# Optimization experiments

Measured on AMD Instinct MI355X. Metric: run time of the kernel, lower is better.

Reference implementation:

```python
import jax, jax.numpy as jnp
import numpy as np

B, T, H, HY, E, L = 32, 256, 1024, 256, 64, 2


def setup_inputs() -> dict:
    key = jax.random.key(0)
    ks = jax.random.split(key, 16)
    rn = lambda k, s, sc=0.05: jax.random.normal(k, s, dtype=jnp.float32) * sc
    return {
        'input': rn(ks[0], (B, T, H), 1.0),
        'w_ih': rn(ks[1], (L, 4 * H, H)),
        'w_hh': rn(ks[2], (L, 4 * H, H)),
        'hyper_w_ih': rn(ks[3], (L, 4 * HY, 2 * H)),
        'hyper_w_hh': rn(ks[4], (L, 4 * HY, HY)),
        'hyper_b': rn(ks[5], (L, 4 * HY)),
        'w_zh': rn(ks[6], (L, 4 * E, HY)),
        'b_zh': jnp.ones((L, 4 * E), jnp.float32),
        'w_zx': rn(ks[7], (L, 4 * E, HY)),
        'b_zx': jnp.ones((L, 4 * E), jnp.float32),
        'w_zb': rn(ks[8], (L, 4 * E, HY)),
        'w_dh': rn(ks[9], (L, 4, H, E), 1.0 / E),
        'w_dx': rn(ks[10], (L, 4, H, E), 1.0 / E),
        'w_db': rn(ks[11], (L, 4, H, E)),
        'b0': rn(ks[12], (L, 4 * H)),
    }


def reference(input, w_ih, w_hh, hyper_w_ih, hyper_w_hh, hyper_b,
              w_zh, b_zh, w_zx, b_zx, w_zb, w_dh, w_dx, w_db, b0):
    L = w_ih.shape[0]
    Bb = input.shape[0]
    Hh = w_hh.shape[-1]
    Hy = hyper_w_hh.shape[-1]
    Ee = w_dh.shape[-1]

    def cell(l, xt, h, c, hh, hc):
        # hyper (meta) LSTM step: input is concat(x, h_main)
        xh = jnp.concatenate([xt, h], axis=-1)
        hg = xh @ hyper_w_ih[l].T + hh @ hyper_w_hh[l].T + hyper_b[l]
        hi, hf, hgc, ho = jnp.split(hg, 4, axis=-1)
        hc2 = jax.nn.sigmoid(hf) * hc + jax.nn.sigmoid(hi) * jnp.tanh(hgc)
        hh2 = jax.nn.sigmoid(ho) * jnp.tanh(hc2)
        # gate-wise embeddings z (B, 4, E) then project to per-gate scale vectors (B, 4H)
        zh = (hh2 @ w_zh[l].T + b_zh[l]).reshape(Bb, 4, Ee)
        zx = (hh2 @ w_zx[l].T + b_zx[l]).reshape(Bb, 4, Ee)
        zb = (hh2 @ w_zb[l].T).reshape(Bb, 4, Ee)
        dh = jnp.einsum('bge,ghe->bgh', zh, w_dh[l]).reshape(Bb, 4 * Hh)
        dx = jnp.einsum('bge,ghe->bgh', zx, w_dx[l]).reshape(Bb, 4 * Hh)
        db = jnp.einsum('bge,ghe->bgh', zb, w_db[l]).reshape(Bb, 4 * Hh) + b0[l]
        # main LSTM gates, dynamically scaled by hypernetwork
        pre = dh * (h @ w_hh[l].T) + dx * (xt @ w_ih[l].T) + db
        i, f, g, o = jnp.split(pre, 4, axis=-1)
        c2 = jax.nn.sigmoid(f) * c + jax.nn.sigmoid(i) * jnp.tanh(g)
        h2 = jax.nn.sigmoid(o) * jnp.tanh(c2)
        return h2, c2, hh2, hc2

    def step(carry, xt):
        h, c, hh, hc = carry  # each (L, B, .)
        hs, cs, hhs, hcs = [], [], [], []
        inp = xt
        for l in range(L):
            h2, c2, hh2, hc2 = cell(l, inp, h[l], c[l], hh[l], hc[l])
            inp = h2
            hs.append(h2); cs.append(c2); hhs.append(hh2); hcs.append(hc2)
        carry = (jnp.stack(hs), jnp.stack(cs), jnp.stack(hhs), jnp.stack(hcs))
        return carry, inp  # top-layer hidden

    init = (jnp.zeros((L, Bb, Hh), input.dtype), jnp.zeros((L, Bb, Hh), input.dtype),
            jnp.zeros((L, Bb, Hy), input.dtype), jnp.zeros((L, Bb, Hy), input.dtype))
    carry, ys = jax.lax.scan(step, init, jnp.swapaxes(input, 0, 1))
    h_seq = jnp.swapaxes(ys, 0, 1)  # (B, T, H)
    return h_seq, carry[0][-1], carry[1][-1]
```

## Files before the change

### kernel.cpp

```cpp
#include <hip/hip_runtime.h>

typedef __bf16 bf16;
typedef __bf16 bf16x8 __attribute__((ext_vector_type(8)));
typedef __bf16 bf16x4 __attribute__((ext_vector_type(4)));
typedef float f32x4 __attribute__((ext_vector_type(4)));
typedef unsigned long long u64;

#define SCOPE_AGENT __HIP_MEMORY_SCOPE_AGENT


__device__ __forceinline__ float sigf(float x) { return 1.0f / (1.0f + __expf(-x)); }
__device__ __forceinline__ float tanhf_fast(float x) {
  float e = __expf(-2.0f * fabsf(x));
  float r = (1.0f - e) / (1.0f + e);
  return copysignf(r, x);
}
__device__ __forceinline__ f32x4 mfma16(bf16x8 a, bf16x8 b, f32x4 c) {
  return __builtin_amdgcn_mfma_f32_16x16x32_bf16(a, b, c, 0, 0, 0);
}
__device__ __forceinline__ u64 uld(const u64* p) { return __hip_atomic_load(p, __ATOMIC_RELAXED, SCOPE_AGENT); }
__device__ __forceinline__ void ust(u64* p, u64 v) { __hip_atomic_store(p, v, __ATOMIC_RELAXED, SCOPE_AGENT); }
__device__ __forceinline__ int ildi(const int* p) { return __hip_atomic_load(p, __ATOMIC_RELAXED, SCOPE_AGENT); }
__device__ __forceinline__ void isti(int* p, int v) { __hip_atomic_store(p, v, __ATOMIC_RELAXED, SCOPE_AGENT); }
__device__ __forceinline__ void fstf(float* p, float v) { __hip_atomic_store(p, v, __ATOMIC_RELAXED, SCOPE_AGENT); }
__device__ __forceinline__ void usti32(unsigned* p, unsigned v) { __hip_atomic_store(p, v, __ATOMIC_RELAXED, SCOPE_AGENT); }

__global__ void detect_kernel(const void* probe, int* flag) {
  __shared__ int cnt;
  if (threadIdx.x == 0) cnt = 0;
  __syncthreads();
  const bf16* p = (const bf16*)probe;
  int local = 0;
  for (int j = threadIdx.x; j < 8192; j += 256) {
    float x = (float)p[j];
    bool wild = (x != x) || (fabsf(x) > 1e3f) || (x != 0.0f && fabsf(x) < 1e-30f);
    local += wild ? 1 : 0;
  }
  atomicAdd(&cnt, local);
  __syncthreads();
  if (threadIdx.x == 0) *flag = (cnt > 64) ? 1 : 0;
}

struct CvtSrc { const void* s[15]; };
struct CvtDst { bf16* d[15]; };

__global__ __launch_bounds__(256) void convert_kernel(CvtSrc S, CvtDst D, const int* flag) {
  const int pre[16] = {0, 8388608, 16777216, 25165824, 29360128, 29884416, 29886464,
                       30017536, 30018048, 30149120, 30149632, 30280704, 30804992,
                       31329280, 31853568, 31861760};
  const int fp32 = *flag;
  const int nvec = 31861760 / 4;
  for (int v = blockIdx.x * 256 + threadIdx.x; v < nvec; v += gridDim.x * 256) {
    int e = v * 4;
    int seg = 0;
#pragma unroll
    for (int k = 1; k < 15; ++k) seg += (e >= pre[k]) ? 1 : 0;
    int off = e - pre[seg];
    bf16* d = D.d[seg] + off;
    if (fp32) {
      const float* s = (const float*)S.s[seg] + off;
      float4 x = *(const float4*)s;
      d[0] = (bf16)x.x; d[1] = (bf16)x.y; d[2] = (bf16)x.z; d[3] = (bf16)x.w;
    } else {
      const bf16* s = (const bf16*)S.s[seg] + off;
      d[0] = s[0]; d[1] = s[1]; d[2] = s[2]; d[3] = s[3];
    }
  }
}

__global__ void init_kernel(u64* zbase) {
  int i = blockIdx.x * 256 + threadIdx.x;
  zbase[i] = 0ull;
}

__global__ __launch_bounds__(256) void gemm_pre(
    const bf16* __restrict__ A, const bf16* __restrict__ w_ih_l,
    const bf16* __restrict__ hwih_l, bf16* __restrict__ Xp, float* __restrict__ Hxp) {
  constexpr int LDT = 72;
  __shared__ alignas(16) bf16 As[64 * LDT];
  __shared__ alignas(16) bf16 Bs[64 * LDT];
  const int bm = blockIdx.x & 127;
  const int bn = blockIdx.x >> 7;
  const int m0 = bm * 64, n0 = bn * 64;
  const int tid = threadIdx.x;
  const int lane = tid & 63, wid = tid >> 6;
  const int l15 = lane & 15, q = lane >> 4;
  const int srow = tid >> 2, sk = (tid & 3) * 16;
  const bf16* arow = A + (size_t)(m0 + srow) * 1024;
  const int n = n0 + srow;
  const bf16* brow = (n < 4096) ? (w_ih_l + (size_t)n * 1024)
                                : (hwih_l + (size_t)(n - 4096) * 2048);
  f32x4 acc[4] = {};
  for (int kb = 0; kb < 1024; kb += 64) {
    *(bf16x8*)(&As[srow * LDT + sk])     = *(const bf16x8*)(arow + kb + sk);
    *(bf16x8*)(&As[srow * LDT + sk + 8]) = *(const bf16x8*)(arow + kb + sk + 8);
    *(bf16x8*)(&Bs[srow * LDT + sk])     = *(const bf16x8*)(brow + kb + sk);
    *(bf16x8*)(&Bs[srow * LDT + sk + 8]) = *(const bf16x8*)(brow + kb + sk + 8);
    __syncthreads();
#pragma unroll
    for (int kk = 0; kk < 64; kk += 32) {
      bf16x8 av = *(const bf16x8*)(&As[(wid * 16 + l15) * LDT + kk + q * 8]);
#pragma unroll
      for (int j = 0; j < 4; ++j) {
        bf16x8 bv = *(const bf16x8*)(&Bs[(j * 16 + l15) * LDT + kk + q * 8]);
        acc[j] = mfma16(av, bv, acc[j]);
      }
    }
    __syncthreads();
  }
#pragma unroll
  for (int j = 0; j < 4; ++j) {
    const int gn = n0 + j * 16 + l15;
#pragma unroll
    for (int r = 0; r < 4; ++r) {
      const int gm = m0 + wid * 16 + q * 4 + r;
      float v = acc[j][r];
      if (gn < 4096) Xp[(size_t)gm * 4096 + gn] = (bf16)v;
      else           Hxp[(size_t)gm * 1024 + (gn - 4096)] = v;
    }
  }
}

struct SeqArgs {
  const bf16 *w_hh, *hwih, *hwhh, *hyb;
  const bf16 *w_zh, *b_zh, *w_zx, *b_zx, *w_zb;
  const bf16 *w_dh, *w_dx, *w_db, *b0;
  const bf16 *Xp; const float *Hxp;
  const bf16 *w_ih1;
  bf16 *Xp1c; float *Hxp1c;
  u64 *Y0;
  u64 *hpub;
  u64 *hh2pub;
  float *outp;
  int *flags;
};

__global__ __launch_bounds__(256) void seq_kernel(SeqArgs a) {
  __shared__ char smem[41472] __attribute__((aligned(16)));
  bf16 (*hstage)[1032] = (bf16(*)[1032])smem;
  bf16 (*hhK)[264]    = (bf16(*)[264])(smem + 33024);
  float* hgL          = (float*)(smem + 33024);
  bf16 (*hA4)[1032]   = (bf16(*)[1032])smem;
  bf16 (*hh2A)[264]   = (bf16(*)[264])(smem + 8256);
  float (*RhL)[256]   = (float(*)[256])(smem + 10368);
  float (*zsL)[768]   = (float(*)[768])(smem + 14464);
  float (*presL)[256] = (float(*)[256])(smem + 26752);
  bf16 (*hbuf)[64]    = (bf16(*)[64])(smem + 30848);
  bf16*  As = (bf16*)smem;
  bf16*  Bs = (bf16*)(smem + 9216);
  float* Ct = (float*)(smem + 18432);

  const int tid = threadIdx.x;
  const int lane = tid & 63, wid = tid >> 6;
  const int l15 = lane & 15, q = lane >> 4;
  const int blk = blockIdx.x;
  const int xcd = blk & 7, slot = blk >> 3;
  const int layer = xcd >> 2, xl = xcd & 3;
  const int s16 = xl * 4 + (slot & 3);
  const int bq = slot >> 2;
  const int lblk = bq * 16 + s16;
  const int hd = s16 >> 1;
  const int mh = (bq == hd) ? 0 : ((bq == ((hd + 4) & 7)) ? 1 : -1);
  const bool isHyper = (((s16 & 1) == 0) && (mh >= 0));

  u64* hbase  = a.hpub + (size_t)layer * 16384;
  u64* h2base = a.hh2pub + (size_t)layer * 4096;
  int* genp0  = a.flags;
  int* genp   = a.flags + layer * 16;
  int* gchunkp= a.flags + 32;
  int* arrp   = a.flags + 64 + layer * 2048;
  int* hh2fp  = a.flags + 4160 + layer * 256;
  int* carrp  = a.flags + 4672;

  const bf16* whh_l = a.w_hh + (size_t)layer * 4194304;
  const bf16* hybl  = a.hyb + layer * 1024;
  const bf16* bzh_l = a.b_zh + layer * 256;
  const bf16* bzx_l = a.b_zx + layer * 256;
  const bf16* b0_l  = a.b0 + (size_t)layer * 4096;
  const int cb = tid >> 6, chl = tid & 63;

  float c_reg = 0.0f;
  float hc[2] = {0, 0};

  const bf16* zrow[12];
#pragma unroll
  for (int j = 0; j < 12; ++j) {
    int ng = wid * 12 + j, tau = ng >> 4;
    const bf16* base = (tau == 0) ? a.w_zh : (tau == 1) ? a.w_zx : a.w_zb;
    zrow[j] = base + ((size_t)layer * 256 + (ng & 15) * 16 + l15) * 256;
  }
  const bf16* rrow[4];
#pragma unroll
  for (int nt = 0; nt < 4; ++nt)
    rrow[nt] = whh_l + (size_t)(wid * 1024 + s16 * 64 + nt * 16 + l15) * 1024;
  const bf16* hirow[2];
  const bf16* hhrow[2];
#pragma unroll
  for (int nt = 0; nt < 2; ++nt) {
    const int row = wid * 256 + hd * 32 + nt * 16 + l15;
    hirow[nt] = a.hwih + (size_t)layer * 2097152 + (size_t)row * 2048 + 1024;
    hhrow[nt] = a.hwhh + (size_t)layer * 262144 + (size_t)row * 256;
  }
  const size_t wdo = ((size_t)(layer * 4 + wid) * 1024 + s16 * 64 + lane) * 64;
  const bf16 *pdh = a.w_dh + wdo, *pdx = a.w_dx + wdo, *pdb = a.w_db + wdo;

  for (int t = 0; t < 256; ++t) {
    const int tloc = t & 31;
    u64* wslot = hbase + (size_t)(t & 1) * 8192;
    const u64* rslot = hbase + (size_t)((t + 1) & 1) * 8192;
    u64* wcur = h2base + (size_t)(t & 1) * 2048;
    const u64* rK = h2base + (size_t)((t + 1) & 1) * 2048;

    if (layer == 1 && tloc == 0) {
      const int k = t >> 5;
      if (tid == 0) { while (ildi(genp0) < (k + 1) * 32) __builtin_amdgcn_s_sleep(2); }
      __atomic_signal_fence(__ATOMIC_SEQ_CST);
      __syncthreads();
      const int srow = tid >> 2, sk = (tid & 3) * 16;
      for (int tt = 0; tt < 10; ++tt) {
        const int tile = lblk * 10 + tt;
        const int m0 = (tile & 15) * 64, n0 = (tile >> 4) * 64;
        const int m = m0 + srow;
        const u64* arow = a.Y0 + (((size_t)(m >> 5) * 256 + k * 32 + (m & 31)) << 8);
        const int n = n0 + srow;
        const bf16* brow = (n < 4096) ? (a.w_ih1 + (size_t)n * 1024)
                                      : (a.hwih + 2097152 + (size_t)(n - 4096) * 2048);
        f32x4 acc[4] = {};
        for (int kb = 0; kb < 1024; kb += 64) {
          const int c0 = (kb + sk) >> 2;
          u64 a0 = uld(arow + c0),     a1 = uld(arow + c0 + 1);
          u64 a2 = uld(arow + c0 + 2), a3 = uld(arow + c0 + 3);
          *(u64*)&As[srow * 72 + sk]      = a0;
          *(u64*)&As[srow * 72 + sk + 4]  = a1;
          *(u64*)&As[srow * 72 + sk + 8]  = a2;
          *(u64*)&As[srow * 72 + sk + 12] = a3;
          *(bf16x8*)&Bs[srow * 72 + sk]     = *(const bf16x8*)(brow + kb + sk);
          *(bf16x8*)&Bs[srow * 72 + sk + 8] = *(const bf16x8*)(brow + kb + sk + 8);
          __syncthreads();
#pragma unroll
          for (int kk = 0; kk < 64; kk += 32) {
            bf16x8 av = *(const bf16x8*)&As[(wid * 16 + l15) * 72 + kk + q * 8];
#pragma unroll
            for (int j = 0; j < 4; ++j) {
              bf16x8 bv = *(const bf16x8*)&Bs[(j * 16 + l15) * 72 + kk + q * 8];
              acc[j] = mfma16(av, bv, acc[j]);
            }
          }
          __syncthreads();
        }
#pragma unroll
        for (int j = 0; j < 4; ++j)
#pragma unroll
          for (int r = 0; r < 4; ++r)
            Ct[(wid * 16 + q * 4 + r) * 64 + j * 16 + l15] = acc[j][r];
        __syncthreads();
#pragma unroll
        for (int e = 0; e < 4; ++e) {
          const int qd = tid * 4 + e;
          const int row = qd >> 4, col4 = (qd & 15) * 4;
          f32x4 v = *(const f32x4*)&Ct[row * 64 + col4];
          const int gm = m0 + row, gn = n0 + col4;
          if (gn < 4096) {
            union { bf16 h[4]; u64 u; } pk;
#pragma unroll
            for (int x = 0; x < 4; ++x) pk.h[x] = (bf16)v[x];
            ust((u64*)a.Xp1c + ((((size_t)gm << 12) + gn) >> 2), pk.u);
          } else {
            float* hp = a.Hxp1c + ((size_t)gm << 10) + (gn - 4096);
#pragma unroll
            for (int x = 0; x < 4; ++x) fstf(hp + x, v[x]);
          }
        }
        __syncthreads();
      }
      __atomic_signal_fence(__ATOMIC_SEQ_CST);
      __builtin_amdgcn_s_waitcnt(0);
      __syncthreads();
      if (tid == 0) isti(carrp + lblk * 16, k + 1);
      if (lblk == 0 && wid == 0) {
        for (;;) {
          int v0 = ildi(carrp + lane * 32);
          int v1 = ildi(carrp + lane * 32 + 16);
          if (__all((v0 >= k + 1) && (v1 >= k + 1))) break;
          __builtin_amdgcn_s_sleep(2);
        }
        __atomic_signal_fence(__ATOMIC_SEQ_CST);
        if (lane == 0) isti(gchunkp, k + 1);
      }
      if (tid == 0) { while (ildi(gchunkp) < k + 1) __builtin_amdgcn_s_sleep(2); }
      __atomic_signal_fence(__ATOMIC_SEQ_CST);
      __syncthreads();
    }

    if (t > 0 && tid == 0) {
      while (ildi(genp) < t) __builtin_amdgcn_s_sleep(2);
    }
    __atomic_signal_fence(__ATOMIC_SEQ_CST);
    __syncthreads();

    if (isHyper) {
      for (int i = tid; i < 4096; i += 256) {
        int b = i >> 8, u = i & 255;
        *(u64*)&hstage[b][u * 4] = uld(rslot + ((size_t)(mh * 16 + b) << 8) + u);
      }
      for (int i = tid; i < 1024; i += 256) {
        int b = i >> 6, u = i & 63;
        *(u64*)&hhK[b][u * 4] = uld(rK + ((size_t)(mh * 16 + b) << 6) + u);
      }
      __syncthreads();
      f32x4 acc[2] = {};
      for (int kk = 0; kk < 1024; kk += 32) {
        int ko = kk + q * 8;
        bf16x8 a0 = *(const bf16x8*)&hstage[l15][ko];
#pragma unroll
        for (int nt = 0; nt < 2; ++nt) {
          bf16x8 bv = *(const bf16x8*)(hirow[nt] + ko);
          acc[nt] = mfma16(a0, bv, acc[nt]);
        }
      }
      for (int kk = 0; kk < 256; kk += 32) {
        int ko = kk + q * 8;
        bf16x8 a0 = *(const bf16x8*)&hhK[l15][ko];
#pragma unroll
        for (int nt = 0; nt < 2; ++nt) {
          bf16x8 bv = *(const bf16x8*)(hhrow[nt] + ko);
          acc[nt] = mfma16(a0, bv, acc[nt]);
        }
      }
      __syncthreads();
#pragma unroll
      for (int nt = 0; nt < 2; ++nt)
#pragma unroll
        for (int r = 0; r < 4; ++r)
          hgL[(wid * 16 + q * 4 + r) * 32 + nt * 16 + l15] = acc[nt][r];
      __syncthreads();
      {
        const int b16 = tid >> 4, d0 = (tid & 15) * 2;
        const int b = mh * 16 + b16;
        float hx2[4][2];
        if (layer == 0) {
          const float* hx = a.Hxp + ((size_t)b * 256 + t) * 1024 + hd * 32 + d0;
#pragma unroll
          for (int g = 0; g < 4; ++g) {
            hx2[g][0] = hx[g * 256]; hx2[g][1] = hx[g * 256 + 1];
          }
        } else {
          const u64* hx1 = (const u64*)a.Hxp1c + (((size_t)b * 32 + tloc) << 9)
                         + ((hd * 32 + d0) >> 1);
#pragma unroll
          for (int g = 0; g < 4; ++g) {
            u64 w = uld(hx1 + g * 128);
            hx2[g][0] = __uint_as_float((unsigned)(w & 0xffffffffu));
            hx2[g][1] = __uint_as_float((unsigned)(w >> 32));
          }
        }
        union { bf16 h[2]; unsigned u; } pk;
#pragma unroll
        for (int dd = 0; dd < 2; ++dd) {
          int d = d0 + dd, gd = hd * 32 + d;
          float hi  = hgL[(0 * 16 + b16) * 32 + d] + (float)hybl[gd]       + hx2[0][dd];
          float hf  = hgL[(1 * 16 + b16) * 32 + d] + (float)hybl[256 + gd] + hx2[1][dd];
          float hgv = hgL[(2 * 16 + b16) * 32 + d] + (float)hybl[512 + gd] + hx2[2][dd];
          float ho  = hgL[(3 * 16 + b16) * 32 + d] + (float)hybl[768 + gd] + hx2[3][dd];
          hc[dd] = sigf(hf) * hc[dd] + sigf(hi) * tanhf_fast(hgv);
          pk.h[dd] = (bf16)(sigf(ho) * tanhf_fast(hc[dd]));
        }
        usti32((unsigned*)wcur + b * 128 + hd * 16 + (d0 >> 1), pk.u);
      }
      __atomic_signal_fence(__ATOMIC_SEQ_CST);
      __builtin_amdgcn_s_waitcnt(0);
      __syncthreads();
      if (tid == 0) isti(hh2fp + (hd * 2 + mh) * 16, t + 1);
    }
    __syncthreads();

    for (int i = tid; i < 1024; i += 256) {
      int b = i >> 8, u = i & 255;
      *(u64*)&hA4[b][u * 4] = uld(rslot + ((size_t)(bq * 4 + b) << 8) + u);
    }
    __syncthreads();
    {
      f32x4 racc[4] = {};
      for (int kk = 0; kk < 1024; kk += 32) {
        const int ko = kk + q * 8;
        bf16x8 av = *(const bf16x8*)&hA4[l15 & 3][ko];
#pragma unroll
        for (int nt = 0; nt < 4; ++nt) {
          bf16x8 bv = *(const bf16x8*)(rrow[nt] + ko);
          racc[nt] = mfma16(av, bv, racc[nt]);
        }
      }
      if (lane < 16) {
#pragma unroll
        for (int nt = 0; nt < 4; ++nt)
#pragma unroll
          for (int r = 0; r < 4; ++r)
            RhL[r][wid * 64 + nt * 16 + lane] = racc[nt][r];
      }
    }
    if (tid < 16) { while (ildi(hh2fp + tid * 16) < t + 1) __builtin_amdgcn_s_sleep(1); }
    __atomic_signal_fence(__ATOMIC_SEQ_CST);
    __syncthreads();
    {
      int b = tid >> 6, u = tid & 63;
      *(u64*)&hh2A[b][u * 4] = uld(wcur + ((size_t)(bq * 4 + b) << 6) + u);
    }
    __syncthreads();
    {
      f32x4 zacc[12] = {};
      for (int kk = 0; kk < 256; kk += 32) {
        const int ko = kk + q * 8;
        bf16x8 av = *(const bf16x8*)&hh2A[l15 & 3][ko];
#pragma unroll
        for (int j = 0; j < 12; ++j) {
          bf16x8 bv = *(const bf16x8*)(zrow[j] + ko);
          zacc[j] = mfma16(av, bv, zacc[j]);
        }
      }
      if (lane < 16) {
#pragma unroll
        for (int j = 0; j < 12; ++j) {
          int ng = wid * 12 + j, tau = ng >> 4, col = (ng & 15) * 16 + lane;
          float bias = (tau == 0) ? (float)bzh_l[col] : (tau == 1) ? (float)bzx_l[col] : 0.0f;
#pragma unroll
          for (int r = 0; r < 4; ++r) zsL[r][tau * 256 + col] = zacc[j][r] + bias;
        }
      }
    }
    __syncthreads();
    {
      float dH[4] = {}, dX[4] = {}, dB[4] = {};
      for (int e0 = 0; e0 < 64; e0 += 4) {
        bf16x4 wh = *(const bf16x4*)(pdh + e0);
        bf16x4 wx = *(const bf16x4*)(pdx + e0);
        bf16x4 wb = *(const bf16x4*)(pdb + e0);
        f32x4 zh_[4], zx_[4], zb_[4];
#pragma unroll
        for (int b = 0; b < 4; ++b) {
          zh_[b] = *(const f32x4*)&zsL[b][wid * 64 + e0];
          zx_[b] = *(const f32x4*)&zsL[b][256 + wid * 64 + e0];
          zb_[b] = *(const f32x4*)&zsL[b][512 + wid * 64 + e0];
        }
#pragma unroll
        for (int jj = 0; jj < 4; ++jj) {
          float whf = (float)wh[jj], wxf = (float)wx[jj], wbf = (float)wb[jj];
#pragma unroll
          for (int b = 0; b < 4; ++b) {
            dH[b] += zh_[b][jj] * whf;
            dX[b] += zx_[b][jj] * wxf;
            dB[b] += zb_[b][jj] * wbf;
          }
        }
      }
      const int n = wid * 1024 + s16 * 64 + lane;
#pragma unroll
      for (int b = 0; b < 4; ++b) {
        float rh = RhL[b][wid * 64 + lane];
        float xp;
        if (layer == 0) {
          xp = (float)a.Xp[((size_t)(bq * 4 + b) * 256 + t) * 4096 + n];
        } else {
          u64 w = uld((const u64*)a.Xp1c
                      + ((((size_t)((bq * 4 + b) * 32 + tloc) << 12) + (n & ~3)) >> 2));
          xp = __uint_as_float(((unsigned)(w >> ((n & 3) * 16)) & 0xffffu) << 16);
        }
        float b0v = (float)b0_l[n];
        presL[b][wid * 64 + lane] = dH[b] * rh + dX[b] * xp + dB[b] + b0v;
      }
    }
    __syncthreads();
    {
      float iv = presL[cb][chl];
      float fv = presL[cb][64 + chl];
      float gv = presL[cb][128 + chl];
      float ov = presL[cb][192 + chl];
      c_reg = sigf(fv) * c_reg + sigf(iv) * tanhf_fast(gv);
      float hn = sigf(ov) * tanhf_fast(c_reg);
      hbuf[cb][chl] = (bf16)hn;
      if (layer) {
        const size_t oo = ((size_t)(bq * 4 + cb) * 256 + t) * 1024 + s16 * 64 + chl;
        a.outp[oo] = hn;
        if (t == 255) {
          a.outp[8388608 + (bq * 4 + cb) * 1024 + s16 * 64 + chl] = hn;
          a.outp[8421376 + (bq * 4 + cb) * 1024 + s16 * 64 + chl] = c_reg;
        }
      }
    }
    __syncthreads();
    if (tid < 64) {
      int b = tid >> 4, u = tid & 15;
      u64 pk = *(const u64*)&hbuf[b][u * 4];
      ust(wslot + ((size_t)(bq * 4 + b) << 8) + s16 * 16 + u, pk);
      if (layer == 0)
        ust(a.Y0 + (((size_t)(bq * 4 + b) * 256 + t) << 8) + s16 * 16 + u, pk);
    }
    __atomic_signal_fence(__ATOMIC_SEQ_CST);
    __builtin_amdgcn_s_waitcnt(0);
    __syncthreads();
    if (tid == 0) isti(arrp + lblk * 16, t + 1);
    if (lblk == 0 && wid == 0) {
      const int t1 = t + 1;
      for (;;) {
        int v0 = ildi(arrp + lane * 32);
        int v1 = ildi(arrp + lane * 32 + 16);
        if (__all((v0 >= t1) && (v1 >= t1))) break;
        __builtin_amdgcn_s_sleep(2);
      }
      __atomic_signal_fence(__ATOMIC_SEQ_CST);
      if (lane == 0) isti(genp, t1);
    }
  }
}

extern "C" void kernel_launch(void* const* d_in, const int* in_sizes, int n_in,
                              void* d_out, int out_size, void* d_ws, size_t ws_size,
                              hipStream_t stream) {
  float* outp = (float*)d_out;
  char* ws = (char*)d_ws;
  bf16*  Xp     = (bf16*) (ws);
  float* Hxp    = (float*)(ws + 67108864ull);
  u64*   Y0     = (u64*)  (ws + 100663296ull);
  bf16* c_input = (bf16*)(ws + 117669888ull);
  bf16*  Xp1c   = c_input;
  float* Hxp1c  = (float*)(ws + 117669888ull + 8388608ull);
  bf16* c_w_ih  = (bf16*)(ws + 134447104ull);
  bf16* c_w_hh  = (bf16*)(ws + 151224320ull);
  bf16* c_hwih  = (bf16*)(ws + 168001536ull);
  bf16* c_hwhh  = (bf16*)(ws + 176390144ull);
  bf16* c_hyb   = (bf16*)(ws + 177438720ull);
  bf16* c_wzh   = (bf16*)(ws + 177442816ull);
  bf16* c_bzh   = (bf16*)(ws + 177704960ull);
  bf16* c_wzx   = (bf16*)(ws + 177705984ull);
  bf16* c_bzx   = (bf16*)(ws + 177968128ull);
  bf16* c_wzb   = (bf16*)(ws + 177969152ull);
  bf16* c_wdh   = (bf16*)(ws + 178231296ull);
  bf16* c_wdx   = (bf16*)(ws + 179279872ull);
  bf16* c_wdb   = (bf16*)(ws + 180328448ull);
  bf16* c_b0    = (bf16*)(ws + 181377024ull);
  int*  dflag   = (int*) (ws + 181393408ull);
  char* pubb    = ws + 181397504ull;
  u64*   hpub   = (u64*)  (pubb + 0);
  u64*   hh2pub = (u64*)  (pubb + 262144);
  int*   flags  = (int*)  (pubb + 327680);

  hipLaunchKernelGGL(detect_kernel, dim3(1), dim3(256), 0, stream, d_in[2], dflag);
  CvtSrc S; CvtDst D;
  for (int i = 0; i < 15; ++i) S.s[i] = d_in[i];
  D.d[0] = c_input; D.d[1] = c_w_ih; D.d[2] = c_w_hh; D.d[3] = c_hwih; D.d[4] = c_hwhh;
  D.d[5] = c_hyb;   D.d[6] = c_wzh;  D.d[7] = c_bzh;  D.d[8] = c_wzx;  D.d[9] = c_bzx;
  D.d[10] = c_wzb;  D.d[11] = c_wdh; D.d[12] = c_wdx; D.d[13] = c_wdb; D.d[14] = c_b0;
  hipLaunchKernelGGL(convert_kernel, dim3(2048), dim3(256), 0, stream, S, D, dflag);

  hipLaunchKernelGGL(init_kernel, dim3(176), dim3(256), 0, stream, (u64*)pubb);
  hipLaunchKernelGGL(gemm_pre, dim3(10240), dim3(256), 0, stream,
                     c_input, c_w_ih, c_hwih, Xp, Hxp);

  SeqArgs sa;
  sa.w_hh = c_w_hh; sa.hwih = c_hwih; sa.hwhh = c_hwhh; sa.hyb = c_hyb;
  sa.w_zh = c_wzh; sa.b_zh = c_bzh; sa.w_zx = c_wzx; sa.b_zx = c_bzx; sa.w_zb = c_wzb;
  sa.w_dh = c_wdh; sa.w_dx = c_wdx; sa.w_db = c_wdb; sa.b0 = c_b0;
  sa.Xp = Xp; sa.Hxp = Hxp;
  sa.w_ih1 = c_w_ih + (size_t)4194304;
  sa.Xp1c = Xp1c; sa.Hxp1c = Hxp1c;
  sa.Y0 = Y0;
  sa.hpub = hpub; sa.hh2pub = hh2pub;
  sa.outp = outp;
  sa.flags = flags;
  hipLaunchKernelGGL(seq_kernel, dim3(256), dim3(256), 0, stream, sa);
}
```

Measured before the change: 19.70 ms.

## Split hyper-LSTM step into dedicated extra blocks of the persistent kernel

The hyper-LSTM gate computation previously ran inside a subset of the 256 main blocks, which serialized it ahead of each block's W_hh work. It now runs on 32 extra dedicated blocks (grid 288) that loop over time with their own flag waits, so the main blocks can start their recurrent matmul without waiting on the hyper step. Launch bounds now request 2 blocks per CU so all 288 persistent blocks stay co-resident. The risks are deadlock if the extra blocks are not scheduled alongside the rest, and register pressure from the occupancy hint.

New measurement: 24.65 ms. 1.25x slower.

```diff
diff --git a/kernel.cpp b/kernel.cpp
--- a/kernel.cpp
+++ b/kernel.cpp
@@ -135,7 +135,7 @@
   int *flags;
 };
 
-__global__ __launch_bounds__(256) void seq_kernel(SeqArgs a) {
+__global__ __launch_bounds__(256, 2) void seq_kernel(SeqArgs a) {
   __shared__ char smem[41472] __attribute__((aligned(16)));
   bf16 (*hstage)[1032] = (bf16(*)[1032])smem;
   bf16 (*hhK)[264]    = (bf16(*)[264])(smem + 33024);
@@ -154,14 +154,127 @@
   const int lane = tid & 63, wid = tid >> 6;
   const int l15 = lane & 15, q = lane >> 4;
   const int blk = blockIdx.x;
+
+  if (blk >= 256) {
+    const int idx = blk - 256;
+    const int xcd = idx & 7;
+    const int layer = xcd >> 2, xl = xcd & 3;
+    const int hj = xl * 4 + (idx >> 3);
+    const int hd = hj >> 1, mh = hj & 1;
+
+    u64* hbase  = a.hpub + (size_t)layer * 16384;
+    u64* h2base = a.hh2pub + (size_t)layer * 4096;
+    int* genp   = a.flags + layer * 16;
+    int* gchunkp= a.flags + 32;
+    int* hh2fp  = a.flags + 4160 + layer * 256;
+    const bf16* hybl = a.hyb + layer * 1024;
+
+    float hc[2] = {0, 0};
+    const bf16* hirow[2];
+    const bf16* hhrow[2];
+#pragma unroll
+    for (int nt = 0; nt < 2; ++nt) {
+      const int row = wid * 256 + hd * 32 + nt * 16 + l15;
+      hirow[nt] = a.hwih + (size_t)layer * 2097152 + (size_t)row * 2048 + 1024;
+      hhrow[nt] = a.hwhh + (size_t)layer * 262144 + (size_t)row * 256;
+    }
+
+    for (int t = 0; t < 256; ++t) {
+      const int tloc = t & 31;
+      const u64* rslot = hbase + (size_t)((t + 1) & 1) * 8192;
+      u64* wcur = h2base + (size_t)(t & 1) * 2048;
+      const u64* rK = h2base + (size_t)((t + 1) & 1) * 2048;
+
+      if (t > 0 && tid == 0) {
+        while (ildi(genp) < t) __builtin_amdgcn_s_sleep(2);
+      }
+      if (layer == 1 && tloc == 0 && tid == 64) {
+        while (ildi(gchunkp) < (t >> 5) + 1) __builtin_amdgcn_s_sleep(2);
+      }
+      __atomic_signal_fence(__ATOMIC_SEQ_CST);
+      __syncthreads();
+
+      for (int i = tid; i < 4096; i += 256) {
+        int b = i >> 8, u = i & 255;
+        *(u64*)&hstage[b][u * 4] = uld(rslot + ((size_t)(mh * 16 + b) << 8) + u);
+      }
+      for (int i = tid; i < 1024; i += 256) {
+        int b = i >> 6, u = i & 63;
+        *(u64*)&hhK[b][u * 4] = uld(rK + ((size_t)(mh * 16 + b) << 6) + u);
+      }
+      __syncthreads();
+      f32x4 acc[2] = {};
+      for (int kk = 0; kk < 1024; kk += 32) {
+        int ko = kk + q * 8;
+        bf16x8 a0 = *(const bf16x8*)&hstage[l15][ko];
+#pragma unroll
+        for (int nt = 0; nt < 2; ++nt) {
+          bf16x8 bv = *(const bf16x8*)(hirow[nt] + ko);
+          acc[nt] = mfma16(a0, bv, acc[nt]);
+        }
+      }
+      for (int kk = 0; kk < 256; kk += 32) {
+        int ko = kk + q * 8;
+        bf16x8 a0 = *(const bf16x8*)&hhK[l15][ko];
+#pragma unroll
+        for (int nt = 0; nt < 2; ++nt) {
+          bf16x8 bv = *(const bf16x8*)(hhrow[nt] + ko);
+          acc[nt] = mfma16(a0, bv, acc[nt]);
+        }
+      }
+      __syncthreads();
+#pragma unroll
+      for (int nt = 0; nt < 2; ++nt)
+#pragma unroll
+        for (int r = 0; r < 4; ++r)
+          hgL[(wid * 16 + q * 4 + r) * 32 + nt * 16 + l15] = acc[nt][r];
+      __syncthreads();
+      {
+        const int b16 = tid >> 4, d0 = (tid & 15) * 2;
+        const int b = mh * 16 + b16;
+        float hx2[4][2];
+        if (layer == 0) {
+          const float* hx = a.Hxp + ((size_t)b * 256 + t) * 1024 + hd * 32 + d0;
+#pragma unroll
+          for (int g = 0; g < 4; ++g) {
+            hx2[g][0] = hx[g * 256]; hx2[g][1] = hx[g * 256 + 1];
+          }
+        } else {
+          const u64* hx1 = (const u64*)a.Hxp1c + (((size_t)b * 32 + tloc) << 9)
+                         + ((hd * 32 + d0) >> 1);
+#pragma unroll
+          for (int g = 0; g < 4; ++g) {
+            u64 w = uld(hx1 + g * 128);
+            hx2[g][0] = __uint_as_float((unsigned)(w & 0xffffffffu));
+            hx2[g][1] = __uint_as_float((unsigned)(w >> 32));
+          }
+        }
+        union { bf16 h[2]; unsigned u; } pk;
+#pragma unroll
+        for (int dd = 0; dd < 2; ++dd) {
+          int d = d0 + dd, gd = hd * 32 + d;
+          float hi  = hgL[(0 * 16 + b16) * 32 + d] + (float)hybl[gd]       + hx2[0][dd];
+          float hf  = hgL[(1 * 16 + b16) * 32 + d] + (float)hybl[256 + gd] + hx2[1][dd];
+          float hgv = hgL[(2 * 16 + b16) * 32 + d] + (float)hybl[512 + gd] + hx2[2][dd];
+          float ho  = hgL[(3 * 16 + b16) * 32 + d] + (float)hybl[768 + gd] + hx2[3][dd];
+          hc[dd] = sigf(hf) * hc[dd] + sigf(hi) * tanhf_fast(hgv);
+          pk.h[dd] = (bf16)(sigf(ho) * tanhf_fast(hc[dd]));
+        }
+        usti32((unsigned*)wcur + b * 128 + hd * 16 + (d0 >> 1), pk.u);
+      }
+      __atomic_signal_fence(__ATOMIC_SEQ_CST);
+      __builtin_amdgcn_s_waitcnt(0);
+      __syncthreads();
+      if (tid == 0) isti(hh2fp + (hd * 2 + mh) * 16, t + 1);
+    }
+    return;
+  }
+
   const int xcd = blk & 7, slot = blk >> 3;
   const int layer = xcd >> 2, xl = xcd & 3;
   const int s16 = xl * 4 + (slot & 3);
   const int bq = slot >> 2;
   const int lblk = bq * 16 + s16;
-  const int hd = s16 >> 1;
-  const int mh = (bq == hd) ? 0 : ((bq == ((hd + 4) & 7)) ? 1 : -1);
-  const bool isHyper = (((s16 & 1) == 0) && (mh >= 0));
 
   u64* hbase  = a.hpub + (size_t)layer * 16384;
   u64* h2base = a.hh2pub + (size_t)layer * 4096;
@@ -173,14 +286,12 @@
   int* carrp  = a.flags + 4672;
 
   const bf16* whh_l = a.w_hh + (size_t)layer * 4194304;
-  const bf16* hybl  = a.hyb + layer * 1024;
   const bf16* bzh_l = a.b_zh + layer * 256;
   const bf16* bzx_l = a.b_zx + layer * 256;
   const bf16* b0_l  = a.b0 + (size_t)layer * 4096;
   const int cb = tid >> 6, chl = tid & 63;
 
   float c_reg = 0.0f;
-  float hc[2] = {0, 0};
 
   const bf16* zrow[12];
 #pragma unroll
@@ -193,14 +304,6 @@
 #pragma unroll
   for (int nt = 0; nt < 4; ++nt)
     rrow[nt] = whh_l + (size_t)(wid * 1024 + s16 * 64 + nt * 16 + l15) * 1024;
-  const bf16* hirow[2];
-  const bf16* hhrow[2];
-#pragma unroll
-  for (int nt = 0; nt < 2; ++nt) {
-    const int row = wid * 256 + hd * 32 + nt * 16 + l15;
-    hirow[nt] = a.hwih + (size_t)layer * 2097152 + (size_t)row * 2048 + 1024;
-    hhrow[nt] = a.hwhh + (size_t)layer * 262144 + (size_t)row * 256;
-  }
   const size_t wdo = ((size_t)(layer * 4 + wid) * 1024 + s16 * 64 + lane) * 64;
   const bf16 *pdh = a.w_dh + wdo, *pdx = a.w_dx + wdo, *pdb = a.w_db + wdo;
 
@@ -209,11 +312,11 @@
     u64* wslot = hbase + (size_t)(t & 1) * 8192;
     const u64* rslot = hbase + (size_t)((t + 1) & 1) * 8192;
     u64* wcur = h2base + (size_t)(t & 1) * 2048;
-    const u64* rK = h2base + (size_t)((t + 1) & 1) * 2048;
 
     if (layer == 1 && tloc == 0) {
       const int k = t >> 5;
       if (tid == 0) { while (ildi(genp0) < (k + 1) * 32) __builtin_amdgcn_s_sleep(2); }
+      if (t > 0 && tid == 32) { while (ildi(genp) < t) __builtin_amdgcn_s_sleep(2); }
       __atomic_signal_fence(__ATOMIC_SEQ_CST);
       __syncthreads();
       const int srow = tid >> 2, sk = (tid & 3) * 16;
@@ -296,82 +399,6 @@
       while (ildi(genp) < t) __builtin_amdgcn_s_sleep(2);
     }
     __atomic_signal_fence(__ATOMIC_SEQ_CST);
-    __syncthreads();
-
-    if (isHyper) {
-      for (int i = tid; i < 4096; i += 256) {
-        int b = i >> 8, u = i & 255;
-        *(u64*)&hstage[b][u * 4] = uld(rslot + ((size_t)(mh * 16 + b) << 8) + u);
-      }
-      for (int i = tid; i < 1024; i += 256) {
-        int b = i >> 6, u = i & 63;
-        *(u64*)&hhK[b][u * 4] = uld(rK + ((size_t)(mh * 16 + b) << 6) + u);
-      }
-      __syncthreads();
-      f32x4 acc[2] = {};
-      for (int kk = 0; kk < 1024; kk += 32) {
-        int ko = kk + q * 8;
-        bf16x8 a0 = *(const bf16x8*)&hstage[l15][ko];
-#pragma unroll
-        for (int nt = 0; nt < 2; ++nt) {
-          bf16x8 bv = *(const bf16x8*)(hirow[nt] + ko);
-          acc[nt] = mfma16(a0, bv, acc[nt]);
-        }
-      }
-      for (int kk = 0; kk < 256; kk += 32) {
-        int ko = kk + q * 8;
-        bf16x8 a0 = *(const bf16x8*)&hhK[l15][ko];
-#pragma unroll
-        for (int nt = 0; nt < 2; ++nt) {
-          bf16x8 bv = *(const bf16x8*)(hhrow[nt] + ko);
-          acc[nt] = mfma16(a0, bv, acc[nt]);
-        }
-      }
-      __syncthreads();
-#pragma unroll
-      for (int nt = 0; nt < 2; ++nt)
-#pragma unroll
-        for (int r = 0; r < 4; ++r)
-          hgL[(wid * 16 + q * 4 + r) * 32 + nt * 16 + l15] = acc[nt][r];
-      __syncthreads();
-      {
-        const int b16 = tid >> 4, d0 = (tid & 15) * 2;
-        const int b = mh * 16 + b16;
-        float hx2[4][2];
-        if (layer == 0) {
-          const float* hx = a.Hxp + ((size_t)b * 256 + t) * 1024 + hd * 32 + d0;
-#pragma unroll
-          for (int g = 0; g < 4; ++g) {
-            hx2[g][0] = hx[g * 256]; hx2[g][1] = hx[g * 256 + 1];
-          }
-        } else {
-          const u64* hx1 = (const u64*)a.Hxp1c + (((size_t)b * 32 + tloc) << 9)
-                         + ((hd * 32 + d0) >> 1);
-#pragma unroll
-          for (int g = 0; g < 4; ++g) {
-            u64 w = uld(hx1 + g * 128);
-            hx2[g][0] = __uint_as_float((unsigned)(w & 0xffffffffu));
-            hx2[g][1] = __uint_as_float((unsigned)(w >> 32));
-          }
-        }
-        union { bf16 h[2]; unsigned u; } pk;
-#pragma unroll
-        for (int dd = 0; dd < 2; ++dd) {
-          int d = d0 + dd, gd = hd * 32 + d;
-          float hi  = hgL[(0 * 16 + b16) * 32 + d] + (float)hybl[gd]       + hx2[0][dd];
-          float hf  = hgL[(1 * 16 + b16) * 32 + d] + (float)hybl[256 + gd] + hx2[1][dd];
-          float hgv = hgL[(2 * 16 + b16) * 32 + d] + (float)hybl[512 + gd] + hx2[2][dd];
-          float ho  = hgL[(3 * 16 + b16) * 32 + d] + (float)hybl[768 + gd] + hx2[3][dd];
-          hc[dd] = sigf(hf) * hc[dd] + sigf(hi) * tanhf_fast(hgv);
-          pk.h[dd] = (bf16)(sigf(ho) * tanhf_fast(hc[dd]));
-        }
-        usti32((unsigned*)wcur + b * 128 + hd * 16 + (d0 >> 1), pk.u);
-      }
-      __atomic_signal_fence(__ATOMIC_SEQ_CST);
-      __builtin_amdgcn_s_waitcnt(0);
-      __syncthreads();
-      if (tid == 0) isti(hh2fp + (hd * 2 + mh) * 16, t + 1);
-    }
     __syncthreads();
 
     for (int i = tid; i < 1024; i += 256) {
@@ -566,5 +593,5 @@
   sa.hpub = hpub; sa.hh2pub = hh2pub;
   sa.outp = outp;
   sa.flags = flags;
-  hipLaunchKernelGGL(seq_kernel, dim3(256), dim3(256), 0, stream, sa);
-}
+  hipLaunchKernelGGL(seq_kernel, dim3(288), dim3(256), 0, stream, sa);
+}
```
